# Kernel tuning notes

Measured on AMD Instinct MI355X. Metric: run time of the kernel, lower is better.

Reference implementation:

```python
import jax, jax.numpy as jnp
import numpy as np

H, HKV, D, HID, T = 16, 4, 128, 2048, 4096
THETA = 10000.0
EPS = 1e-5
NEG = -1e30


def setup_inputs() -> dict:
    key = jax.random.key(0)
    ks = jax.random.split(key, 4)
    return {
        "positions": jnp.arange(T, dtype=jnp.int32),
        "hidden_states": jax.random.normal(ks[0], (T, HID), jnp.float32),
        "w_qkv": jax.random.normal(ks[1], ((H + 2 * HKV) * D, HID), jnp.float32) * 0.02,
        "w_o": jax.random.normal(ks[2], (HID, H * D), jnp.float32) * 0.02,
        "q_norm_w": jnp.ones((H * D,), jnp.float32),
        "k_norm_w": jnp.ones((HKV * D,), jnp.float32),
    }


def _rope(pos, x):
    # x: [T, nh, D]; neox-style rotary over full head_dim
    half = D // 2
    inv_freq = 1.0 / (THETA ** (jnp.arange(0, D, 2, dtype=jnp.float32) / D))  # [D/2]
    ang = pos.astype(jnp.float32)[:, None] * inv_freq  # [T, D/2]
    cos = jnp.cos(ang)[:, None, :]
    sin = jnp.sin(ang)[:, None, :]
    x1, x2 = x[..., :half], x[..., half:]
    return jnp.concatenate([x1 * cos - x2 * sin, x2 * cos + x1 * sin], axis=-1)


def _rmsnorm(x, w):
    var = jnp.mean(x * x, axis=-1, keepdims=True)
    return x * jax.lax.rsqrt(var + EPS) * w


def reference(positions, hidden_states, w_qkv, w_o, q_norm_w, k_norm_w):
    qkv = hidden_states @ w_qkv.T  # [T, (H+2*HKV)*D]
    q, k, v = jnp.split(qkv, [H * D, H * D + HKV * D], axis=-1)
    # RoPE per head
    q = _rope(positions, q.reshape(T, H, D)).reshape(T, H * D)
    k = _rope(positions, k.reshape(T, HKV, D)).reshape(T, HKV * D)
    # QK-norm over the flattened (all-heads) q_size / kv_size, as in the module
    q = _rmsnorm(q, q_norm_w)
    k = _rmsnorm(k, k_norm_w)
    qh = q.reshape(T, H, D)
    kh = jnp.repeat(k.reshape(T, HKV, D), H // HKV, axis=1)  # GQA expand
    vh = jnp.repeat(v.reshape(T, HKV, D), H // HKV, axis=1)
    scores = jnp.einsum('qhd,khd->hqk', qh, kh) * (D ** -0.5)  # [H, T, T]
    causal = jnp.tril(jnp.ones((T, T), dtype=bool))
    scores = jnp.where(causal, scores, NEG)
    p = jax.nn.softmax(scores, axis=-1)
    attn = jnp.einsum('hqk,khd->qhd', p, vh).reshape(T, H * D)
    return attn @ w_o.T  # [T, HID]
```

## Files before the change

### kernel.cpp

```cpp
#include <hip/hip_runtime.h>
#include <hip/hip_bf16.h>

#define T_SEQ 4096
#define HID   2048
#define NH    16
#define NKV   4
#define HD    128
#define QKV_N 3072
#define QSCALE 0.12751744f
#define SMAX 24.0f

typedef unsigned short u16;
typedef __bf16 bf16x8 __attribute__((ext_vector_type(8)));
typedef float floatx4 __attribute__((ext_vector_type(4)));
typedef float floatx16 __attribute__((ext_vector_type(16)));

__device__ __forceinline__ float b2f(u16 u) {
  union { unsigned int i; float f; } x; x.i = ((unsigned int)u) << 16; return x.f;
}
__device__ __forceinline__ u16 f2b(float f) {
  union { float f; unsigned int i; } x; x.f = f;
  unsigned int i = x.i;
  unsigned int r = (i + 0x7FFFu + ((i >> 16) & 1u)) >> 16;
  return (u16)r;
}
__device__ __forceinline__ void gload_lds16(const u16* g, u16* lds) {
  __builtin_amdgcn_global_load_lds(
      (const __attribute__((address_space(1))) unsigned int*)g,
      (__attribute__((address_space(3))) unsigned int*)lds, 16, 0, 0);
}

__global__ __launch_bounds__(256) void conv_f32_bf16(const float* __restrict__ src,
                                                     u16* __restrict__ dst, int n8) {
  int i = blockIdx.x * 256 + threadIdx.x;
  if (i >= n8) return;
  const float4* s = (const float4*)(src + (size_t)i * 8);
  float4 a = s[0], b = s[1];
  union { u16 h[8]; uint4 u; } r;
  r.h[0] = f2b(a.x); r.h[1] = f2b(a.y); r.h[2] = f2b(a.z); r.h[3] = f2b(a.w);
  r.h[4] = f2b(b.x); r.h[5] = f2b(b.y); r.h[6] = f2b(b.z); r.h[7] = f2b(b.w);
  *(uint4*)(dst + (size_t)i * 8) = r.u;
}

template <int CF>
__global__ __launch_bounds__(256) void gemm_bt(const u16* __restrict__ A, int lda,
                                               const u16* __restrict__ B, int ldb,
                                               void* __restrict__ Cv, int ldc, int K) {
  __shared__ __align__(16) u16 sA[2][128 * 64];
  __shared__ __align__(16) u16 sB[2][128 * 64];
  const int tid = threadIdx.x;
  const int wave = tid >> 6, lane = tid & 63;
  const int row0 = blockIdx.y * 128, col0 = blockIdx.x * 128;
  const int wm = (wave >> 1) * 64, wn = (wave & 1) * 64;
  const int frow = lane & 15;
  const int fkb = (lane >> 4) * 16;

  floatx4 acc[4][4];
#pragma unroll
  for (int i = 0; i < 4; i++)
#pragma unroll
    for (int j = 0; j < 4; j++) acc[i][j] = (floatx4){0.f, 0.f, 0.f, 0.f};

  const u16* gA[4];
  const u16* gB[4];
  int doff[4];
#pragma unroll
  for (int p = 0; p < 4; p++) {
    int d = (p * 256 + tid) * 16;
    int row = d >> 7;
    int c = (d & 127) ^ ((row & 7) << 4);
    gA[p] = A + (size_t)(row0 + row) * lda + (c >> 1);
    gB[p] = B + (size_t)(col0 + row) * ldb + (c >> 1);
    doff[p] = (p * 256 + wave * 64) * 8;
  }

#pragma unroll
  for (int p = 0; p < 4; p++) {
    gload_lds16(gA[p], &sA[0][0] + doff[p]);
    gload_lds16(gB[p], &sB[0][0] + doff[p]);
  }
  __syncthreads();
  int cur = 0;
  for (int k0 = 0; k0 < K; k0 += 64) {
    if (k0 + 64 < K) {
      u16* san = &sA[cur ^ 1][0];
      u16* sbn = &sB[cur ^ 1][0];
#pragma unroll
      for (int p = 0; p < 4; p++) {
        gload_lds16(gA[p] + k0 + 64, san + doff[p]);
        gload_lds16(gB[p] + k0 + 64, sbn + doff[p]);
      }
    }
    const u16* pa = &sA[cur][0];
    const u16* pb = &sB[cur][0];
#pragma unroll
    for (int kk = 0; kk < 2; kk++) {
      bf16x8 af[4], bfv[4];
#pragma unroll
      for (int i = 0; i < 4; i++) {
        int rowA = wm + i * 16 + frow;
        int bA = (rowA * 128 + kk * 64 + fkb) ^ ((rowA & 7) << 4);
        af[i] = *(const bf16x8*)(pa + (bA >> 1));
        int rowB = wn + i * 16 + frow;
        int bB = (rowB * 128 + kk * 64 + fkb) ^ ((rowB & 7) << 4);
        bfv[i] = *(const bf16x8*)(pb + (bB >> 1));
      }
#pragma unroll
      for (int i = 0; i < 4; i++)
#pragma unroll
        for (int j = 0; j < 4; j++)
          acc[i][j] = __builtin_amdgcn_mfma_f32_16x16x32_bf16(af[i], bfv[j], acc[i][j], 0, 0, 0);
    }
    __syncthreads();
    cur ^= 1;
  }
  const int crow = (lane >> 4) * 4, ccol = lane & 15;
#pragma unroll
  for (int i = 0; i < 4; i++)
#pragma unroll
    for (int j = 0; j < 4; j++)
#pragma unroll
      for (int r = 0; r < 4; r++) {
        int rr = row0 + wm + i * 16 + crow + r;
        int cc = col0 + wn + j * 16 + ccol;
        if (CF) ((float*)Cv)[(size_t)rr * ldc + cc] = acc[i][j][r];
        else    ((u16*)Cv)[(size_t)rr * ldc + cc] = f2b(acc[i][j][r]);
      }
}

__device__ __forceinline__ void fast_sincos(float ang, float* s, float* c) {
  float r = ang * 0.15915494309189535f;
  r -= floorf(r);
  *s = __builtin_amdgcn_sinf(r);
  *c = __builtin_amdgcn_cosf(r);
}

__global__ __launch_bounds__(256) void rope_norm(const int* __restrict__ pos_arr,
                                                 u16* __restrict__ qkv,
                                                 const float* __restrict__ qnw,
                                                 const float* __restrict__ knw) {
  const int t = blockIdx.x;
  const int tid = threadIdx.x;
  const int lane = tid & 63, wave = tid >> 6;
  u16* row = qkv + (size_t)t * QKV_N;
  const float pos = (float)pos_arr[t];

  float qv[8];
  float ssq = 0.f;
#pragma unroll
  for (int i = 0; i < 8; i++) {
    int e = tid * 8 + i;
    int r = e & 127, ih = e & 63;
    float invf = exp2f(-(float)ih * 0.20762050593046015f);
    float ang = pos * invf;
    float s, c;
    fast_sincos(ang, &s, &c);
    float val;
    if (r < 64) val = b2f(row[e]) * c - b2f(row[e + 64]) * s;
    else        val = b2f(row[e]) * c + b2f(row[e - 64]) * s;
    qv[i] = val;
    ssq += val * val;
  }
  float kv[2];
  float ssk = 0.f;
  const u16* krow = row + HID;
#pragma unroll
  for (int i = 0; i < 2; i++) {
    int e = tid * 2 + i;
    int r = e & 127, ih = e & 63;
    float invf = exp2f(-(float)ih * 0.20762050593046015f);
    float ang = pos * invf;
    float s, c;
    fast_sincos(ang, &s, &c);
    float val;
    if (r < 64) val = b2f(krow[e]) * c - b2f(krow[e + 64]) * s;
    else        val = b2f(krow[e]) * c + b2f(krow[e - 64]) * s;
    kv[i] = val;
    ssk += val * val;
  }
#pragma unroll
  for (int off = 1; off < 64; off <<= 1) {
    ssq += __shfl_xor(ssq, off);
    ssk += __shfl_xor(ssk, off);
  }
  __shared__ float rq[4], rk[4];
  if (lane == 0) { rq[wave] = ssq; rk[wave] = ssk; }
  __syncthreads();
  float sq = rq[0] + rq[1] + rq[2] + rq[3];
  float sk = rk[0] + rk[1] + rk[2] + rk[3];
  float qsc = rsqrtf(sq * (1.0f / 2048.0f) + 1e-5f) * QSCALE;
  float ksc = rsqrtf(sk * (1.0f / 512.0f) + 1e-5f);
#pragma unroll
  for (int i = 0; i < 8; i++) {
    int e = tid * 8 + i;
    row[e] = f2b(qv[i] * qsc * qnw[e]);
  }
#pragma unroll
  for (int i = 0; i < 2; i++) {
    int e = tid * 2 + i;
    row[HID + e] = f2b(kv[i] * ksc * knw[e]);
  }
}

__global__ __launch_bounds__(256) void transpose_v(const u16* __restrict__ qkv,
                                                   u16* __restrict__ vt) {
  __shared__ __align__(16) u16 tile[64][136];
  const int tid = threadIdx.x;
  const int h = blockIdx.y;
  const int t0 = blockIdx.x * 64;
#pragma unroll
  for (int p = 0; p < 4; p++) {
    int v = p * 256 + tid;
    int r = v >> 4, c = v & 15;
    const u16* g = qkv + (size_t)(t0 + r) * QKV_N + (HID + NKV * HD) + h * HD + c * 8;
    *(uint4*)(&tile[r][c * 8]) = *(const uint4*)g;
  }
  __syncthreads();
#pragma unroll
  for (int p = 0; p < 4; p++) {
    int v = p * 256 + tid;
    int d = v >> 3, c8 = v & 7;
    union { u16 s[8]; uint4 q; } tmp;
#pragma unroll
    for (int i = 0; i < 8; i++) tmp.s[i] = tile[c8 * 8 + i][d];
    u16* g = vt + ((size_t)h * HD + d) * T_SEQ + t0 + c8 * 8;
    *(uint4*)g = tmp.q;
  }
}

__device__ __forceinline__ void stage_kv(const u16* __restrict__ kbase,
                                         const u16* __restrict__ vbase, int kv0,
                                         u16* sk, u16* sv, int tid) {
  const int w = tid >> 6, lane = tid & 63;
#pragma unroll
  for (int i = 0; i < 4; i++) {
    int c = w * 256 + i * 64 + lane;
    int kv = c >> 4, ch = c & 15;
    const u16* g = kbase + (size_t)(kv0 + kv) * QKV_N + ((ch ^ (kv & 7)) * 8);
    gload_lds16(g, sk + (size_t)(w * 256 + i * 64) * 8);
  }
#pragma unroll
  for (int i = 0; i < 4; i++) {
    int c = w * 256 + i * 64 + lane;
    int d = c >> 3, c2 = c & 7;
    const u16* g = vbase + (size_t)d * T_SEQ + kv0 + ((c2 ^ (d & 7)) * 8);
    gload_lds16(g, sv + (size_t)(w * 256 + i * 64) * 8);
  }
}

__global__ __launch_bounds__(256, 2) void attn_kernel(u16* __restrict__ qkv,
                                                      const u16* __restrict__ vt,
                                                      float* __restrict__ scratch,
                                                      float* __restrict__ lbuf) {
  __shared__ __align__(16) u16 sK[2][64 * 128];
  __shared__ __align__(16) u16 sV[2][128 * 64];
  const int tid = threadIdx.x;
  const int wave = tid >> 6, lane = tid & 63;
  const int bid = blockIdx.x;

  const int x = bid & 7, slot = bid >> 3;
  int h, qt, part = 0;
  bool split;
  if (slot < 80) {
    const int pr = slot / 10, r = slot - pr * 10;
    if (r < 4)      { qt = 31 - 2 * pr; part = r & 1;       h = 2 * x + (r >> 1);       split = true;  }
    else if (r < 6) { qt = 15 - pr;                         h = 2 * x + (r - 4);        split = false; }
    else            { qt = 30 - 2 * pr; part = (r - 6) & 1; h = 2 * x + ((r - 6) >> 1); split = true;  }
  } else {
    const int j = slot - 80;
    qt = 7 - (j >> 1);
    h = 2 * x + (j & 1);
    split = false;
  }
  const int s_begin = (split && part) ? (qt + 1) : 0;
  const int s_end   = split ? (part ? 2 * (qt + 1) : (qt + 1)) : 2 * (qt + 1);

  const int kvh = h >> 2;
  const int ql = lane & 31;
  const int fq2 = lane >> 5;
  const u16* kbase = qkv + HID + (size_t)kvh * HD;
  const u16* vbase = vt + (size_t)kvh * HD * T_SEQ;

  const int qw = qt * 128 + wave * 32;
  const int qmax = qw + 31;
  const int qrow = qw + ql;
  bf16x8 qf[8];
  const u16* qp = qkv + (size_t)qrow * QKV_N + h * HD + fq2 * 8;
#pragma unroll
  for (int kc = 0; kc < 8; kc++) qf[kc] = *(const bf16x8*)(qp + kc * 16);
  floatx16 O[4];
#pragma unroll
  for (int dt = 0; dt < 4; dt++)
#pragma unroll
    for (int r = 0; r < 16; r++) O[dt][r] = 0.f;
  float l_part = 0.f;

  const int nsteps = s_end - s_begin;
  stage_kv(kbase, vbase, s_begin * 64, sK[0], sV[0], tid);
#pragma unroll 1
  for (int st = 0; st < nsteps; st++) {
    const int s = s_begin + st;
    __syncthreads();
    if (st + 1 < nsteps)
      stage_kv(kbase, vbase, (s + 1) * 64, sK[(st + 1) & 1], sV[(st + 1) & 1], tid);
    const int kv0 = s * 64;
    if (kv0 <= qmax) {
      const u16* sk = sK[st & 1];
      const u16* sv = sV[st & 1];
      const int ntv = (kv0 + 32 <= qmax) ? 2 : 1;
#pragma unroll
      for (int nt = 0; nt < 2; nt++) {
        if (nt < ntv) {
          floatx16 S;
#pragma unroll
          for (int r = 0; r < 16; r++) S[r] = -SMAX;
          __builtin_amdgcn_s_setprio(1);
#pragma unroll
          for (int kc = 0; kc < 8; kc++) {
            int ch = (kc * 2 + fq2) ^ (ql & 7);
            bf16x8 kf = *(const bf16x8*)(sk + ((nt * 32 + ql) * 16 + ch) * 8);
            S = __builtin_amdgcn_mfma_f32_32x32x16_bf16(kf, qf[kc], S, 0, 0, 0);
          }
          __builtin_amdgcn_s_setprio(0);
          const bool tmask = (kv0 + nt * 32 + 31) > qw;
#pragma unroll
          for (int r = 0; r < 16; r++) {
            float v = S[r];
            if (tmask) {
              int kvg = kv0 + nt * 32 + (r & 3) + ((r >> 2) << 3) + (fq2 << 2);
              v = (kvg > qrow) ? -1e30f : v;
            }
            float p = __builtin_amdgcn_exp2f(v);
            l_part += p;
            S[r] = p;
          }
          unsigned cp[8];
#pragma unroll
          for (int i = 0; i < 8; i++) {
            unsigned wv;
            asm("v_cvt_pk_bf16_f32 %0, %1, %2"
                : "=v"(wv) : "v"(S[i * 2]), "v"(S[i * 2 + 1]));
            cp[i] = wv;
          }
          union { unsigned u[4]; bf16x8 v; } pf0, pf1;
          {
            auto r0 = __builtin_amdgcn_permlane32_swap(cp[0], cp[2], false, false);
            pf0.u[0] = r0[0]; pf0.u[2] = r0[1];
            auto r1 = __builtin_amdgcn_permlane32_swap(cp[1], cp[3], false, false);
            pf0.u[1] = r1[0]; pf0.u[3] = r1[1];
            auto r2 = __builtin_amdgcn_permlane32_swap(cp[4], cp[6], false, false);
            pf1.u[0] = r2[0]; pf1.u[2] = r2[1];
            auto r3 = __builtin_amdgcn_permlane32_swap(cp[5], cp[7], false, false);
            pf1.u[1] = r3[0]; pf1.u[3] = r3[1];
          }
          __builtin_amdgcn_s_setprio(1);
#pragma unroll
          for (int c = 0; c < 2; c++) {
            bf16x8 pf = c ? pf1.v : pf0.v;
#pragma unroll
            for (int dt = 0; dt < 4; dt++) {
              int ch2 = ((nt * 2 + c) * 2 + fq2) ^ (ql & 7);
              bf16x8 vf = *(const bf16x8*)(sv + ((dt * 32 + ql) * 8 + ch2) * 8);
              O[dt] = __builtin_amdgcn_mfma_f32_32x32x16_bf16(vf, pf, O[dt], 0, 0, 0);
            }
          }
          __builtin_amdgcn_s_setprio(0);
        }
      }
    }
  }
  float l = l_part + __shfl_xor(l_part, 32);
  if (!split) {
    float inv = 1.0f / fmaxf(l, 1e-30f);
    u16* orow = qkv + (size_t)qrow * QKV_N + h * HD;
#pragma unroll
    for (int dt = 0; dt < 4; dt++)
#pragma unroll
      for (int rg = 0; rg < 4; rg++) {
        union { u16 hh[4]; uint2 uu; } wv;
#pragma unroll
        for (int rr = 0; rr < 4; rr++) wv.hh[rr] = f2b(O[dt][rg * 4 + rr] * inv);
        *(uint2*)(orow + dt * 32 + rg * 8 + fq2 * 4) = wv.uu;
      }
  } else {
    const int tile = h * 16 + (qt - 16);
    float* obase = scratch + (size_t)(part * 256 + tile) * 16384 +
                   (size_t)(wave * 32 + ql) * 128;
#pragma unroll
    for (int dt = 0; dt < 4; dt++)
#pragma unroll
      for (int rg = 0; rg < 4; rg++) {
        float4 wv = {O[dt][rg * 4 + 0], O[dt][rg * 4 + 1],
                     O[dt][rg * 4 + 2], O[dt][rg * 4 + 3]};
        *(float4*)(obase + dt * 32 + rg * 8 + fq2 * 4) = wv;
      }
    if (fq2 == 0) lbuf[(part * 256 + tile) * 128 + wave * 32 + ql] = l;
  }
}

__global__ __launch_bounds__(256) void combine_split(const float* __restrict__ scratch,
                                                     const float* __restrict__ lbuf,
                                                     u16* __restrict__ qkv) {
  const int t = blockIdx.x;
  const int h = t >> 4, qt = 16 + (t & 15);
  const int tid = threadIdx.x;
  const int rsub = tid >> 4;
  const int d0 = (tid & 15) * 8;
  const float* s0 = scratch + (size_t)t * 16384;
  const float* s1 = scratch + (size_t)(256 + t) * 16384;
#pragma unroll
  for (int p = 0; p < 8; p++) {
    int r = p * 16 + rsub;
    float l0 = lbuf[t * 128 + r];
    float l1 = lbuf[32768 + t * 128 + r];
    float inv = 1.0f / fmaxf(l0 + l1, 1e-30f);
    const float4* a4 = (const float4*)(s0 + (size_t)r * 128 + d0);
    const float4* b4 = (const float4*)(s1 + (size_t)r * 128 + d0);
    float4 a0 = a4[0], a1 = a4[1];
    float4 b0 = b4[0], b1 = b4[1];
    union { u16 hh[8]; uint4 u; } wv;
    wv.hh[0] = f2b((a0.x + b0.x) * inv); wv.hh[1] = f2b((a0.y + b0.y) * inv);
    wv.hh[2] = f2b((a0.z + b0.z) * inv); wv.hh[3] = f2b((a0.w + b0.w) * inv);
    wv.hh[4] = f2b((a1.x + b1.x) * inv); wv.hh[5] = f2b((a1.y + b1.y) * inv);
    wv.hh[6] = f2b((a1.z + b1.z) * inv); wv.hh[7] = f2b((a1.w + b1.w) * inv);
    *(uint4*)(qkv + (size_t)(qt * 128 + r) * QKV_N + h * HD + d0) = wv.u;
  }
}

extern "C" void kernel_launch(void* const* d_in, const int* in_sizes, int n_in,
                              void* d_out, int out_size, void* d_ws, size_t ws_size,
                              hipStream_t stream) {
  const int* positions = (const int*)d_in[0];
  const float* hidden = (const float*)d_in[1];
  const float* w_qkv = (const float*)d_in[2];
  const float* w_o = (const float*)d_in[3];
  const float* qnw = (const float*)d_in[4];
  const float* knw = (const float*)d_in[5];
  float* out = (float*)d_out;

  u16* qkv  = (u16*)d_ws;
  u16* bufA = qkv + (size_t)T_SEQ * QKV_N;
  u16* bufB = bufA + (size_t)T_SEQ * HID;
  float* lbuf = (float*)(bufB + 2097152);
  float* scratch = out;

  conv_f32_bf16<<<4096, 256, 0, stream>>>(hidden, bufA, T_SEQ * HID / 8);
  conv_f32_bf16<<<3072, 256, 0, stream>>>(w_qkv, bufB, QKV_N * HID / 8);
  gemm_bt<0><<<dim3(QKV_N / 128, T_SEQ / 128), 256, 0, stream>>>(
      bufA, HID, bufB, HID, qkv, QKV_N, HID);
  rope_norm<<<T_SEQ, 256, 0, stream>>>(positions, qkv, qnw, knw);
  conv_f32_bf16<<<2048, 256, 0, stream>>>(w_o, bufA, HID * HID / 8);
  transpose_v<<<dim3(T_SEQ / 64, NKV), 256, 0, stream>>>(qkv, bufB);
  attn_kernel<<<768, 256, 0, stream>>>(qkv, bufB, scratch, lbuf);
  combine_split<<<256, 256, 0, stream>>>(scratch, lbuf, qkv);
  gemm_bt<1><<<dim3(HID / 128, T_SEQ / 128), 256, 0, stream>>>(
      qkv, QKV_N, bufA, HID, out, HID, HID);
}
```

Baseline: 366.5 us.

## Use 256x256 tile GEMM with 512 threads for QKV projection

Adds a new bf16 GEMM kernel with 256x256 output tiles, 8 waves per block, swizzled LDS via direct global-to-LDS loads, and split A-fragment loads interleaved with next-tile prefetch. Only the QKV projection uses it. Larger tiles raise arithmetic intensity and cut redundant global traffic. The cost is 128KB of LDS per block and fewer blocks (192) on the device, which may leave CUs underused.

```diff
diff --git a/kernel.cpp b/kernel.cpp
--- a/kernel.cpp
+++ b/kernel.cpp
@@ -40,6 +40,135 @@
   r.h[0] = f2b(a.x); r.h[1] = f2b(a.y); r.h[2] = f2b(a.z); r.h[3] = f2b(a.w);
   r.h[4] = f2b(b.x); r.h[5] = f2b(b.y); r.h[6] = f2b(b.z); r.h[7] = f2b(b.w);
   *(uint4*)(dst + (size_t)i * 8) = r.u;
+}
+
+template <int CF>
+__global__ __launch_bounds__(512, 2) void gemm_bt256(const u16* __restrict__ A, int lda,
+                                                     const u16* __restrict__ B, int ldb,
+                                                     void* __restrict__ Cv, int ldc, int K) {
+  __shared__ __align__(16) u16 sA[2][256 * 64];
+  __shared__ __align__(16) u16 sB[2][256 * 64];
+  const int tid = threadIdx.x;
+  const int wave = tid >> 6, lane = tid & 63;
+  const int wr = wave >> 2, wc = wave & 3;
+  const int row0 = blockIdx.y * 256, col0 = blockIdx.x * 256;
+  const int frow = lane & 15;
+  const int fk16 = (lane >> 4) * 16;
+
+  floatx4 acc[8][4];
+#pragma unroll
+  for (int i = 0; i < 8; i++)
+#pragma unroll
+    for (int j = 0; j < 4; j++) acc[i][j] = (floatx4){0.f, 0.f, 0.f, 0.f};
+
+  const u16* gA[4];
+  const u16* gB[4];
+  int doff[4];
+#pragma unroll
+  for (int j = 0; j < 4; j++) {
+    int idx = j * 512 + tid;
+    int row = idx >> 3;
+    int cb = (idx & 7) * 16;
+    int scb = cb ^ ((row & 7) << 4);
+    gA[j] = A + (size_t)(row0 + row) * lda + (scb >> 1);
+    gB[j] = B + (size_t)(col0 + row) * ldb + (scb >> 1);
+    doff[j] = (j * 512 + wave * 64) * 8;
+  }
+
+#pragma unroll
+  for (int j = 0; j < 4; j++) gload_lds16(gB[j], &sB[0][0] + doff[j]);
+  gload_lds16(gA[0], &sA[0][0] + doff[0]);
+  gload_lds16(gA[2], &sA[0][0] + doff[2]);
+  gload_lds16(gA[1], &sA[0][0] + doff[1]);
+  gload_lds16(gA[3], &sA[0][0] + doff[3]);
+#pragma unroll
+  for (int j = 0; j < 4; j++) { gA[j] += 64; gB[j] += 64; }
+
+  const int nt = K >> 6;
+  int cur = 0;
+  for (int t = 0; t < nt; ++t) {
+    asm volatile("s_waitcnt vmcnt(2)" ::: "memory");
+    __builtin_amdgcn_s_barrier();
+    __builtin_amdgcn_sched_barrier(0);
+    const u16* pa = &sA[cur][0];
+    const u16* pb = &sB[cur][0];
+    u16* san = &sA[cur ^ 1][0];
+    u16* sbn = &sB[cur ^ 1][0];
+    const bool more = (t + 1 < nt);
+    if (more) {
+#pragma unroll
+      for (int j = 0; j < 4; j++) gload_lds16(gB[j], sbn + doff[j]);
+    }
+    bf16x8 bfr[4][2];
+#pragma unroll
+    for (int j = 0; j < 4; j++)
+#pragma unroll
+      for (int kk = 0; kk < 2; kk++) {
+        int rowB = wc * 64 + j * 16 + frow;
+        int cbB = (kk * 64 + fk16) ^ ((rowB & 7) << 4);
+        bfr[j][kk] = *(const bf16x8*)(pb + rowB * 64 + (cbB >> 1));
+      }
+    bf16x8 afr[4][2];
+#pragma unroll
+    for (int i = 0; i < 4; i++)
+#pragma unroll
+      for (int kk = 0; kk < 2; kk++) {
+        int rowA = wr * 128 + i * 16 + frow;
+        int cbA = (kk * 64 + fk16) ^ ((rowA & 7) << 4);
+        afr[i][kk] = *(const bf16x8*)(pa + rowA * 64 + (cbA >> 1));
+      }
+    __builtin_amdgcn_s_setprio(1);
+#pragma unroll
+    for (int i = 0; i < 4; i++)
+#pragma unroll
+      for (int j = 0; j < 4; j++)
+#pragma unroll
+        for (int kk = 0; kk < 2; kk++)
+          acc[i][j] = __builtin_amdgcn_mfma_f32_16x16x32_bf16(afr[i][kk], bfr[j][kk], acc[i][j], 0, 0, 0);
+    __builtin_amdgcn_s_setprio(0);
+    if (more) asm volatile("s_waitcnt vmcnt(4)" ::: "memory");
+    else      asm volatile("s_waitcnt vmcnt(0)" ::: "memory");
+    __builtin_amdgcn_s_barrier();
+    __builtin_amdgcn_sched_barrier(0);
+    if (more) {
+      gload_lds16(gA[0], san + doff[0]);
+      gload_lds16(gA[2], san + doff[2]);
+      gload_lds16(gA[1], san + doff[1]);
+      gload_lds16(gA[3], san + doff[3]);
+#pragma unroll
+      for (int j = 0; j < 4; j++) { gA[j] += 64; gB[j] += 64; }
+    }
+#pragma unroll
+    for (int i = 0; i < 4; i++)
+#pragma unroll
+      for (int kk = 0; kk < 2; kk++) {
+        int rowA = wr * 128 + 64 + i * 16 + frow;
+        int cbA = (kk * 64 + fk16) ^ ((rowA & 7) << 4);
+        afr[i][kk] = *(const bf16x8*)(pa + rowA * 64 + (cbA >> 1));
+      }
+    __builtin_amdgcn_s_setprio(1);
+#pragma unroll
+    for (int i = 0; i < 4; i++)
+#pragma unroll
+      for (int j = 0; j < 4; j++)
+#pragma unroll
+        for (int kk = 0; kk < 2; kk++)
+          acc[i + 4][j] = __builtin_amdgcn_mfma_f32_16x16x32_bf16(afr[i][kk], bfr[j][kk], acc[i + 4][j], 0, 0, 0);
+    __builtin_amdgcn_s_setprio(0);
+    cur ^= 1;
+  }
+  const int crow = (lane >> 4) * 4, ccol = lane & 15;
+#pragma unroll
+  for (int i = 0; i < 8; i++)
+#pragma unroll
+    for (int j = 0; j < 4; j++)
+#pragma unroll
+      for (int r = 0; r < 4; r++) {
+        int rr = row0 + wr * 128 + i * 16 + crow + r;
+        int cc = col0 + wc * 64 + j * 16 + ccol;
+        if (CF) ((float*)Cv)[(size_t)rr * ldc + cc] = acc[i][j][r];
+        else    ((u16*)Cv)[(size_t)rr * ldc + cc] = f2b(acc[i][j][r]);
+      }
 }
 
 template <int CF>
@@ -446,7 +575,7 @@
 
   conv_f32_bf16<<<4096, 256, 0, stream>>>(hidden, bufA, T_SEQ * HID / 8);
   conv_f32_bf16<<<3072, 256, 0, stream>>>(w_qkv, bufB, QKV_N * HID / 8);
-  gemm_bt<0><<<dim3(QKV_N / 128, T_SEQ / 128), 256, 0, stream>>>(
+  gemm_bt256<0><<<dim3(QKV_N / 256, T_SEQ / 256), 512, 0, stream>>>(
       bufA, HID, bufB, HID, qkv, QKV_N, HID);
   rope_norm<<<T_SEQ, 256, 0, stream>>>(positions, qkv, qnw, knw);
   conv_f32_bf16<<<2048, 256, 0, stream>>>(w_o, bufA, HID * HID / 8);
```

Measured after the change: 369.9 us. Within noise of the previous version (+0.9%).
